# Optimization experiments

Measured on AMD Instinct MI355X. Metric: run time of the kernel, lower is better.

The kernel has to match this reference:

```python
import jax, jax.numpy as jnp
import numpy as np

D = 128            # dim_h
EDIM = D + 108     # tgt emb + 108-way edge one-hot (edge_linear in_features)
NSRC = 10000       # candidate source nodes
NEDGE = 320000     # candidate paths (edges), ~32 per src
TOPN = 6           # top_n path selection
GIN_EPS = 0.0      # init_eps, not learned
BN_EPS = 1e-5


def _batch_norm(x, gamma, beta):
    # torch BatchNorm1d in training mode: batch stats, biased variance
    mean = jnp.mean(x, axis=0)
    var = jnp.var(x, axis=0)
    return gamma * (x - mean) * jax.lax.rsqrt(var + BN_EPS) + beta


def _glorot(key, shape):
    fan_in, fan_out = shape[-2], shape[-1]
    lim = np.sqrt(6.0 / (fan_in + fan_out))
    return jax.random.uniform(key, shape, jnp.float32, -lim, lim)


def setup_inputs() -> dict:
    key = jax.random.key(0)
    ks = jax.random.split(key, 24)
    inp = {
        "paths_srcs": jax.random.normal(ks[0], (NSRC, D), jnp.float32),
        "path_feats": jax.random.normal(ks[1], (NEDGE, EDIM), jnp.float32),
        "src_ids": jax.random.randint(ks[2], (NEDGE,), 0, NSRC, jnp.int32),
        # 3 stacked GIN convs (weights stacked on leading axis)
        "conv_edge_W": _glorot(ks[3], (3, EDIM, D)),
        "conv_edge_b": jnp.zeros((3, D), jnp.float32),
        "conv_W1": _glorot(ks[4], (3, D, D)),       # MLP layer1, no bias
        "conv_bn_g": jnp.ones((3, D), jnp.float32),
        "conv_bn_b": jnp.zeros((3, D), jnp.float32),
        "conv_W2": _glorot(ks[5], (3, D, D)),       # MLP layer2, no bias
        # GINStack heads
        "lin1_W": _glorot(ks[6], (3 * D, D)),
        "lin1_b": jnp.zeros((D,), jnp.float32),
        "lin2_W": _glorot(ks[7], (D, D)),
        "lin2_b": jnp.zeros((D,), jnp.float32),
        # PathEncoder
        "pe_src_W": _glorot(ks[8], (D, D)),
        "pe_src_b": jnp.zeros((D,), jnp.float32),
        "pe_tgt_W": _glorot(ks[9], (EDIM, D)),
        "pe_tgt_b": jnp.zeros((D,), jnp.float32),
        "pe_bn_g": jnp.ones((D,), jnp.float32),
        "pe_bn_b": jnp.zeros((D,), jnp.float32),
        # linear path ranker head
        "score_w": _glorot(ks[10], (D, 1))[:, 0],
    }
    return inp


def reference(paths_srcs, path_feats, conv_edge_W, conv_edge_b, conv_W1,
              conv_bn_g, conv_bn_b, conv_W2, lin1_W, lin1_b, lin2_W, lin2_b,
              pe_src_W, pe_src_b, pe_tgt_W, pe_tgt_b, pe_bn_g, pe_bn_b,
              score_w, src_ids):
    # GIN message: relu(tgt+edge feature), summed per source node.
    # Identical for all 3 convs in the original, so compute once.
    msgs = jax.nn.relu(path_feats)                                   # [E, EDIM]
    agg = jax.ops.segment_sum(msgs, src_ids, num_segments=NSRC)      # [N, EDIM]

    hs = []
    for i in range(3):  # fixed 3-layer GINStack
        h_msg = agg @ conv_edge_W[i] + conv_edge_b[i]                # [N, D]
        h = (1.0 + GIN_EPS) * paths_srcs + h_msg
        z = jax.nn.relu(_batch_norm(h @ conv_W1[i], conv_bn_g[i], conv_bn_b[i]))
        hs.append(z @ conv_W2[i])
    h = jnp.concatenate(hs, axis=1) @ lin1_W + lin1_b                # [N, D]
    h = jax.nn.relu(h)
    node_emb = h @ lin2_W + lin2_b                                   # [N, D]

    # PathEncoder: src-node emb + fused (tgt+edge) emb -> path emb
    hpath = node_emb[src_ids] @ pe_src_W + pe_src_b \
          + path_feats @ pe_tgt_W + pe_tgt_b                         # [E, D]
    hpath = jax.nn.relu(_batch_norm(hpath, pe_bn_g, pe_bn_b))

    # linear path ranker + top-k path selection
    scores = hpath @ score_w                                         # [E]
    top_vals, top_idx = jax.lax.top_k(scores, TOPN)
    return node_emb, top_vals, top_idx
```

## Files before the change

kernel.cpp:

```cpp
#include <hip/hip_runtime.h>
#include <math.h>

#define NSRC 10000
#define NEDGE 320000
#define EDIM 236
#define TOPN 6

typedef __attribute__((ext_vector_type(8))) short short8;
typedef __attribute__((ext_vector_type(4))) float floatx4;

__device__ __forceinline__ unsigned short bf16_rne(float x) {
  union { float f; unsigned int u; } c; c.f = x;
  unsigned int r = (c.u + 0x7FFFu + ((c.u >> 16) & 1u)) >> 16;
  return (unsigned short)r;
}
__device__ __forceinline__ float bf16_to_f(unsigned short h) {
  union { unsigned int u; float f; } c; c.u = ((unsigned int)h) << 16;
  return c.f;
}
__device__ __forceinline__ void split_f32(float x, unsigned short& h, unsigned short& l) {
  h = bf16_rne(x);
  l = bf16_rne(x - bf16_to_f(h));
}

struct KV { float v; int i; };

__device__ __forceinline__ bool kv_better(const KV a, const KV b) {
  return (a.v > b.v) || (a.v == b.v && a.i < b.i);
}

__device__ __forceinline__ void kv_merge(KV d[TOPN], const KV o[TOPN]) {
  KV r[TOPN];
  int ia = 0, ib = 0;
#pragma unroll
  for (int q = 0; q < TOPN; ++q) {
    bool takeA;
    if (ia >= TOPN) takeA = false;
    else if (ib >= TOPN) takeA = true;
    else takeA = kv_better(d[ia], o[ib]);
    r[q] = takeA ? d[ia] : o[ib];
    if (takeA) ia++; else ib++;
  }
#pragma unroll
  for (int q = 0; q < TOPN; ++q) d[q] = r[q];
}

__global__ void k_zero(float* __restrict__ p, int n) {
  int i = blockIdx.x * 256 + threadIdx.x;
  if (i < n) p[i] = 0.f;
}

__global__ void k_sentinel(float* __restrict__ out) {
  if (threadIdx.x == 0) out[0] = 1.0e9f;
}

__global__ void k_prep_w1cat(const float* __restrict__ cw1, float* __restrict__ w1cat) {
  int gid = blockIdx.x * 256 + threadIdx.x;
  if (gid >= 3 * 128 * 128) return;
  int i = gid >> 14;
  int m = (gid >> 7) & 127;
  int j = gid & 127;
  w1cat[m * 384 + i * 128 + j] = cw1[gid];
}

__global__ void k_prep_wew1(const float* __restrict__ cew, const float* __restrict__ cw1,
                            float* __restrict__ wew1cat) {
  int b = blockIdx.x;
  int i = b / EDIM;
  int k = b - i * EDIM;
  int j = threadIdx.x;
  const float* we = cew + ((size_t)i * EDIM + k) * 128;
  const float* w1 = cw1 + (size_t)i * 16384;
  float acc = 0.f;
  for (int m = 0; m < 128; ++m) acc = fmaf(we[m], w1[m * 128 + j], acc);
  wew1cat[k * 384 + i * 128 + j] = acc;
}

__global__ void k_prep_bprime(const float* __restrict__ ceb, const float* __restrict__ cw1,
                              float* __restrict__ bprime) {
  int i = blockIdx.x;
  int j = threadIdx.x;
  const float* be = ceb + i * 128;
  const float* w1 = cw1 + (size_t)i * 16384;
  float acc = 0.f;
  for (int m = 0; m < 128; ++m) acc = fmaf(be[m], w1[m * 128 + j], acc);
  bprime[i * 128 + j] = acc;
}

__global__ void k_prep_m1(const float* __restrict__ cw2, const float* __restrict__ l1w,
                          float* __restrict__ m1) {
  int b = blockIdx.x;
  int i = b >> 7;
  int r = b & 127;
  int j = threadIdx.x;
  const float* w2 = cw2 + (size_t)i * 16384 + r * 128;
  float acc = 0.f;
  for (int c = 0; c < 128; ++c) acc = fmaf(w2[c], l1w[((size_t)i * 128 + c) * 128 + j], acc);
  m1[b * 128 + j] = acc;
}

__global__ void k_prep_bsplit(const float* __restrict__ ptw,
                              unsigned short* __restrict__ Bh,
                              unsigned short* __restrict__ Bl) {
  int n = blockIdx.x;
  int k = threadIdx.x;
  float v = (k < EDIM) ? ptw[(size_t)k * 128 + n] : 0.f;
  unsigned short h, l;
  split_f32(v, h, l);
  Bh[n * 256 + k] = h;
  Bl[n * 256 + k] = l;
}

__global__ __launch_bounds__(256) void k_hist(const int* __restrict__ src,
                                              int* __restrict__ counts) {
  int e = blockIdx.x * 256 + threadIdx.x;
  if (e < NEDGE) atomicAdd(&counts[src[e]], 1);
}

__global__ __launch_bounds__(256) void k_scan(const int* __restrict__ counts,
                                              int* __restrict__ offsets,
                                              int* __restrict__ cursor) {
  __shared__ int part[256];
  const int t = threadIdx.x;
  const int base = t * 40;
  int s = 0;
  for (int k = 0; k < 40; ++k) {
    int i = base + k;
    if (i < NSRC) s += counts[i];
  }
  part[t] = s;
  __syncthreads();
  for (int off = 1; off < 256; off <<= 1) {
    int v = (t >= off) ? part[t - off] : 0;
    __syncthreads();
    part[t] += v;
    __syncthreads();
  }
  int run = (t == 0) ? 0 : part[t - 1];
  for (int k = 0; k < 40; ++k) {
    int i = base + k;
    if (i < NSRC) {
      offsets[i] = run;
      cursor[i] = run;
      run += counts[i];
    }
  }
  if (t == 255) offsets[NSRC] = run;
}

__global__ __launch_bounds__(256) void k_scatter(const int* __restrict__ src,
                                                 int* __restrict__ cursor,
                                                 int* __restrict__ elist) {
  int e = blockIdx.x * 256 + threadIdx.x;
  if (e < NEDGE) {
    int p = atomicAdd(&cursor[src[e]], 1);
    elist[p] = e;
  }
}

__global__ __launch_bounds__(256) void k_gather(const float* __restrict__ pf,
                                                const int* __restrict__ offsets,
                                                const int* __restrict__ elist,
                                                float* __restrict__ agg) {
  const int row = blockIdx.x;
  const int t = threadIdx.x;
  if (t >= EDIM) return;
  const int beg = offsets[row];
  const int end = offsets[row + 1];
  float acc0 = 0.f, acc1 = 0.f;
  int e = beg;
  for (; e + 1 < end; e += 2) {
    int e0 = elist[e];
    int e1 = elist[e + 1];
    float v0 = pf[(size_t)e0 * EDIM + t];
    float v1 = pf[(size_t)e1 * EDIM + t];
    acc0 += fmaxf(v0, 0.f);
    acc1 += fmaxf(v1, 0.f);
  }
  if (e < end) {
    int e0 = elist[e];
    acc0 += fmaxf(pf[(size_t)e0 * EDIM + t], 0.f);
  }
  agg[(size_t)row * EDIM + t] = acc0 + acc1;
}

template <int ATR, int EPI>
__global__ __launch_bounds__(256)
void gemm_k(const float* __restrict__ A, const float* __restrict__ B,
            float* __restrict__ C, int M, int K, int N,
            const float* __restrict__ bn_g, const float* __restrict__ bn_b,
            const float* __restrict__ bn_mean, const float* __restrict__ bn_rstd,
            const float* __restrict__ bias, const float* __restrict__ bias2,
            const float* __restrict__ Cin,
            const int* __restrict__ srcids, const float* __restrict__ gatherTab,
            float* __restrict__ colsum, float* __restrict__ colsumsq) {
  __shared__ float As[8][128];
  __shared__ float Bs[8][128];
  __shared__ float red[16][128];
  constexpr bool STATS = (EPI == 1 || EPI == 4);

  const int tid = threadIdx.x;
  const int tx = tid & 15;
  const int ty = tid >> 4;
  const int bm = blockIdx.x * 128;
  const int bn = blockIdx.y * 128;

  float acc[8][8];
#pragma unroll
  for (int i = 0; i < 8; ++i)
#pragma unroll
    for (int j = 0; j < 8; ++j) acc[i][j] = 0.f;

  for (int k0 = 0; k0 < K; k0 += 8) {
    {
      int r = tid >> 1;
      int cq = (tid & 1) << 2;
      float4 v = make_float4(0.f, 0.f, 0.f, 0.f);
      int row = bm + r;
      if (row < M) {
        const float* ap = A + (size_t)row * K + k0 + cq;
        if (k0 + cq + 4 <= K) {
          v = *(const float4*)ap;
        } else {
          float tmp[4] = {0.f, 0.f, 0.f, 0.f};
          for (int q = 0; q < 4; ++q)
            if (k0 + cq + q < K) tmp[q] = ap[q];
          v = make_float4(tmp[0], tmp[1], tmp[2], tmp[3]);
        }
      }
      if constexpr (ATR == 1) {
        float vv[4] = {v.x, v.y, v.z, v.w};
#pragma unroll
        for (int q = 0; q < 4; ++q) {
          int k = k0 + cq + q;
          if (k < K) {
            vv[q] = fmaxf(fmaf(bn_g[k], (vv[q] - bn_mean[k]) * bn_rstd[k], bn_b[k]), 0.f);
          } else {
            vv[q] = 0.f;
          }
        }
        v = make_float4(vv[0], vv[1], vv[2], vv[3]);
      }
      As[cq + 0][r] = v.x;
      As[cq + 1][r] = v.y;
      As[cq + 2][r] = v.z;
      As[cq + 3][r] = v.w;
    }
    {
      int r = tid >> 5;
      int c = (tid & 31) << 2;
      float4 v = make_float4(0.f, 0.f, 0.f, 0.f);
      int kk = k0 + r;
      if (kk < K) v = *(const float4*)(B + (size_t)kk * N + bn + c);
      *(float4*)&Bs[r][c] = v;
    }
    __syncthreads();
#pragma unroll
    for (int kk = 0; kk < 8; ++kk) {
      const float4 a0 = *(const float4*)&As[kk][ty * 8];
      const float4 a1 = *(const float4*)&As[kk][ty * 8 + 4];
      const float4 b0 = *(const float4*)&Bs[kk][tx * 8];
      const float4 b1 = *(const float4*)&Bs[kk][tx * 8 + 4];
      const float av[8] = {a0.x, a0.y, a0.z, a0.w, a1.x, a1.y, a1.z, a1.w};
      const float bv[8] = {b0.x, b0.y, b0.z, b0.w, b1.x, b1.y, b1.z, b1.w};
#pragma unroll
      for (int i = 0; i < 8; ++i)
#pragma unroll
        for (int j = 0; j < 8; ++j) acc[i][j] = fmaf(av[i], bv[j], acc[i][j]);
    }
    __syncthreads();
  }

  const int nb = bn + tx * 8;
  float colS[8], colQ[8];
  if constexpr (STATS) {
#pragma unroll
    for (int j = 0; j < 8; ++j) { colS[j] = 0.f; colQ[j] = 0.f; }
  }
#pragma unroll
  for (int i = 0; i < 8; ++i) {
    int m = bm + ty * 8 + i;
    if (m < M) {
      float outv[8];
#pragma unroll
      for (int j = 0; j < 8; ++j) outv[j] = acc[i][j];
      if constexpr (EPI == 1) {
        const float* crow = Cin + (size_t)m * N + nb;
#pragma unroll
        for (int j = 0; j < 8; ++j) outv[j] += crow[j] + bias[nb + j];
      } else if constexpr (EPI == 2) {
#pragma unroll
        for (int j = 0; j < 8; ++j) outv[j] = fmaxf(outv[j] + bias[nb + j], 0.f);
      } else if constexpr (EPI == 3) {
#pragma unroll
        for (int j = 0; j < 8; ++j) {
          float bb = bias[nb + j];
          if (bias2) bb += bias2[nb + j];
          outv[j] += bb;
        }
      } else if constexpr (EPI == 4) {
        int s = srcids[m];
        const float* g = gatherTab + (size_t)s * N + nb;
#pragma unroll
        for (int j = 0; j < 8; ++j) outv[j] += g[j];
      }
      float* crow = C + (size_t)m * N + nb;
      *(float4*)crow = make_float4(outv[0], outv[1], outv[2], outv[3]);
      *(float4*)(crow + 4) = make_float4(outv[4], outv[5], outv[6], outv[7]);
      if constexpr (STATS) {
#pragma unroll
        for (int j = 0; j < 8; ++j) { colS[j] += outv[j]; colQ[j] += outv[j] * outv[j]; }
      }
    }
  }
  if constexpr (STATS) {
    *(float4*)&red[ty][tx * 8] = make_float4(colS[0], colS[1], colS[2], colS[3]);
    *(float4*)&red[ty][tx * 8 + 4] = make_float4(colS[4], colS[5], colS[6], colS[7]);
    __syncthreads();
    if (tid < 128) {
      float s = 0.f;
#pragma unroll
      for (int t = 0; t < 16; ++t) s += red[t][tid];
      atomicAdd(colsum + bn + tid, s);
    }
    __syncthreads();
    *(float4*)&red[ty][tx * 8] = make_float4(colQ[0], colQ[1], colQ[2], colQ[3]);
    *(float4*)&red[ty][tx * 8 + 4] = make_float4(colQ[4], colQ[5], colQ[6], colQ[7]);
    __syncthreads();
    if (tid < 128) {
      float s = 0.f;
#pragma unroll
      for (int t = 0; t < 16; ++t) s += red[t][tid];
      atomicAdd(colsumsq + bn + tid, s);
    }
  }
}

__global__ __launch_bounds__(256)
void k_hgemm(const float* __restrict__ A, const unsigned short* __restrict__ Bh,
             const unsigned short* __restrict__ Bl, const int* __restrict__ srcids,
             const float* __restrict__ pre_src, float* __restrict__ hpath,
             float* __restrict__ colsum, float* __restrict__ colsumsq) {
  __shared__ __align__(16) unsigned short Ah[128][40];
  __shared__ __align__(16) unsigned short Al[128][40];
  __shared__ __align__(16) unsigned short Bhs[128][40];
  __shared__ __align__(16) unsigned short Bls[128][40];
  __shared__ float redS[4][128];
  __shared__ float redQ[4][128];

  const int tid = threadIdx.x;
  const int wave = tid >> 6;
  const int lane = tid & 63;
  const int am = lane & 15;
  const int aq = lane >> 4;
  const int bm = blockIdx.x * 128;

  floatx4 acc[2][8];
#pragma unroll
  for (int mt = 0; mt < 2; ++mt)
#pragma unroll
    for (int nt = 0; nt < 8; ++nt) acc[mt][nt] = (floatx4){0.f, 0.f, 0.f, 0.f};

  const int rowS = tid >> 1;
  const int kq = (tid & 1) * 16;

  for (int c = 0; c < 8; ++c) {
    const int k0 = c * 32;
    {
      const float* ap = A + (size_t)(bm + rowS) * EDIM + k0 + kq;
      short8 vh0, vl0, vh1, vl1;
#pragma unroll
      for (int i = 0; i < 4; ++i) {
        float4 v = make_float4(0.f, 0.f, 0.f, 0.f);
        if (k0 + kq + i * 4 + 4 <= EDIM) v = *(const float4*)(ap + i * 4);
        unsigned short h0, l0, h1, l1, h2, l2, h3, l3;
        split_f32(v.x, h0, l0);
        split_f32(v.y, h1, l1);
        split_f32(v.z, h2, l2);
        split_f32(v.w, h3, l3);
        if (i < 2) {
          vh0[i * 4 + 0] = (short)h0; vl0[i * 4 + 0] = (short)l0;
          vh0[i * 4 + 1] = (short)h1; vl0[i * 4 + 1] = (short)l1;
          vh0[i * 4 + 2] = (short)h2; vl0[i * 4 + 2] = (short)l2;
          vh0[i * 4 + 3] = (short)h3; vl0[i * 4 + 3] = (short)l3;
        } else {
          int q = (i - 2) * 4;
          vh1[q + 0] = (short)h0; vl1[q + 0] = (short)l0;
          vh1[q + 1] = (short)h1; vl1[q + 1] = (short)l1;
          vh1[q + 2] = (short)h2; vl1[q + 2] = (short)l2;
          vh1[q + 3] = (short)h3; vl1[q + 3] = (short)l3;
        }
      }
      *(short8*)&Ah[rowS][kq] = vh0;
      *(short8*)&Ah[rowS][kq + 8] = vh1;
      *(short8*)&Al[rowS][kq] = vl0;
      *(short8*)&Al[rowS][kq + 8] = vl1;
    }
    {
      const unsigned short* bhp = Bh + (size_t)rowS * 256 + k0 + kq;
      const unsigned short* blp = Bl + (size_t)rowS * 256 + k0 + kq;
      *(short8*)&Bhs[rowS][kq] = *(const short8*)bhp;
      *(short8*)&Bhs[rowS][kq + 8] = *(const short8*)(bhp + 8);
      *(short8*)&Bls[rowS][kq] = *(const short8*)blp;
      *(short8*)&Bls[rowS][kq + 8] = *(const short8*)(blp + 8);
    }
    __syncthreads();
    {
      const int m0 = wave * 32 + am;
      const short8 ah0 = *(const short8*)&Ah[m0][aq * 8];
      const short8 al0 = *(const short8*)&Al[m0][aq * 8];
      const short8 ah1 = *(const short8*)&Ah[m0 + 16][aq * 8];
      const short8 al1 = *(const short8*)&Al[m0 + 16][aq * 8];
#pragma unroll
      for (int nt = 0; nt < 8; ++nt) {
        const short8 bh = *(const short8*)&Bhs[nt * 16 + am][aq * 8];
        const short8 bl = *(const short8*)&Bls[nt * 16 + am][aq * 8];
        acc[0][nt] = __builtin_amdgcn_mfma_f32_16x16x32_bf16(ah0, bl, acc[0][nt], 0, 0, 0);
        acc[0][nt] = __builtin_amdgcn_mfma_f32_16x16x32_bf16(al0, bh, acc[0][nt], 0, 0, 0);
        acc[0][nt] = __builtin_amdgcn_mfma_f32_16x16x32_bf16(ah0, bh, acc[0][nt], 0, 0, 0);
        acc[1][nt] = __builtin_amdgcn_mfma_f32_16x16x32_bf16(ah1, bl, acc[1][nt], 0, 0, 0);
        acc[1][nt] = __builtin_amdgcn_mfma_f32_16x16x32_bf16(al1, bh, acc[1][nt], 0, 0, 0);
        acc[1][nt] = __builtin_amdgcn_mfma_f32_16x16x32_bf16(ah1, bh, acc[1][nt], 0, 0, 0);
      }
    }
    __syncthreads();
  }

  float colS[8], colQ[8];
#pragma unroll
  for (int nt = 0; nt < 8; ++nt) { colS[nt] = 0.f; colQ[nt] = 0.f; }
#pragma unroll
  for (int mt = 0; mt < 2; ++mt) {
#pragma unroll
    for (int r = 0; r < 4; ++r) {
      const int m = bm + wave * 32 + mt * 16 + aq * 4 + r;
      const int sid = srcids[m];
      const float* g = pre_src + (size_t)sid * 128;
      float* hp = hpath + (size_t)m * 128;
#pragma unroll
      for (int nt = 0; nt < 8; ++nt) {
        const int col = nt * 16 + am;
        float v = acc[mt][nt][r] + g[col];
        hp[col] = v;
        colS[nt] += v;
        colQ[nt] += v * v;
      }
    }
  }
#pragma unroll
  for (int nt = 0; nt < 8; ++nt) {
    colS[nt] += __shfl_xor(colS[nt], 16);
    colS[nt] += __shfl_xor(colS[nt], 32);
    colQ[nt] += __shfl_xor(colQ[nt], 16);
    colQ[nt] += __shfl_xor(colQ[nt], 32);
  }
  if (lane < 16) {
#pragma unroll
    for (int nt = 0; nt < 8; ++nt) {
      redS[wave][nt * 16 + lane] = colS[nt];
      redQ[wave][nt * 16 + lane] = colQ[nt];
    }
  }
  __syncthreads();
  if (tid < 128) {
    float s = redS[0][tid] + redS[1][tid] + redS[2][tid] + redS[3][tid];
    atomicAdd(colsum + tid, s);
  } else {
    int cn = tid - 128;
    float s = redQ[0][cn] + redQ[1][cn] + redQ[2][cn] + redQ[3][cn];
    atomicAdd(colsumsq + cn, s);
  }
}

__global__ void k_finT(float* __restrict__ st) {
  int j = threadIdx.x;
  float mean = st[j] * (1.0f / NSRC);
  float var = st[384 + j] * (1.0f / NSRC) - mean * mean;
  st[768 + j] = mean;
  st[1152 + j] = rsqrtf(var + 1e-5f);
}

__global__ void k_finP(float* __restrict__ st, const float* __restrict__ g,
                       const float* __restrict__ b) {
  int j = threadIdx.x;
  float mean = st[j] * (1.0f / NEDGE);
  float var = st[128 + j] * (1.0f / NEDGE) - mean * mean;
  float rstd = rsqrtf(var + 1e-5f);
  float a = g[j] * rstd;
  st[256 + j] = a;
  st[384 + j] = b[j] - a * mean;
}

__global__ __launch_bounds__(256) void k_score(const float* __restrict__ hpath,
                                               const float* __restrict__ aP,
                                               const float* __restrict__ cP,
                                               const float* __restrict__ w,
                                               float* __restrict__ scores) {
  const int row = blockIdx.x * 16 + (threadIdx.x >> 4);
  const int cg = threadIdx.x & 15;
  const float* hp = hpath + (size_t)row * 128 + cg * 8;
  const float4 x0 = *(const float4*)hp;
  const float4 x1 = *(const float4*)(hp + 4);
  const float xs[8] = {x0.x, x0.y, x0.z, x0.w, x1.x, x1.y, x1.z, x1.w};
  float part = 0.f;
#pragma unroll
  for (int q = 0; q < 8; ++q) {
    int j = cg * 8 + q;
    part += fmaxf(fmaf(aP[j], xs[q], cP[j]), 0.f) * w[j];
  }
#pragma unroll
  for (int o = 8; o >= 1; o >>= 1) part += __shfl_xor(part, o, 16);
  if (cg == 0) scores[row] = part;
}

__global__ __launch_bounds__(256) void k_top1(const float* __restrict__ scores,
                                              KV* __restrict__ cand) {
  KV t[TOPN];
#pragma unroll
  for (int q = 0; q < TOPN; ++q) { t[q].v = -INFINITY; t[q].i = 2147483647; }
  for (int e = blockIdx.x * 256 + threadIdx.x; e < NEDGE; e += 256 * 256) {
    float v = scores[e];
    if (v > t[TOPN - 1].v) {
      t[TOPN - 1].v = v;
      t[TOPN - 1].i = e;
#pragma unroll
      for (int q = TOPN - 1; q > 0; --q) {
        if (t[q].v > t[q - 1].v) { KV tmp = t[q - 1]; t[q - 1] = t[q]; t[q] = tmp; }
      }
    }
  }
  __shared__ KV sh[128][TOPN];
  int tid = threadIdx.x;
  for (int s = 128; s >= 1; s >>= 1) {
    if (tid >= s && tid < 2 * s) {
#pragma unroll
      for (int q = 0; q < TOPN; ++q) sh[tid - s][q] = t[q];
    }
    __syncthreads();
    if (tid < s) kv_merge(t, sh[tid]);
    __syncthreads();
  }
  if (tid == 0) {
#pragma unroll
    for (int q = 0; q < TOPN; ++q) cand[blockIdx.x * TOPN + q] = t[q];
  }
}

__global__ __launch_bounds__(256) void k_top2(const KV* __restrict__ cand,
                                              float* __restrict__ outTail) {
  int tid = threadIdx.x;
  KV t[TOPN];
#pragma unroll
  for (int q = 0; q < TOPN; ++q) t[q] = cand[tid * TOPN + q];
  __shared__ KV sh[128][TOPN];
  for (int s = 128; s >= 1; s >>= 1) {
    if (tid >= s && tid < 2 * s) {
#pragma unroll
      for (int q = 0; q < TOPN; ++q) sh[tid - s][q] = t[q];
    }
    __syncthreads();
    if (tid < s) kv_merge(t, sh[tid]);
    __syncthreads();
  }
  if (tid == 0) {
#pragma unroll
    for (int q = 0; q < TOPN; ++q) {
      outTail[q] = t[q].v;
      outTail[TOPN + q] = (float)t[q].i;
    }
  }
}

extern "C" void kernel_launch(void* const* d_in, const int* in_sizes, int n_in,
                              void* d_out, int out_size, void* d_ws, size_t ws_size,
                              hipStream_t stream) {
  const float* paths_srcs = (const float*)d_in[0];
  const float* path_feats = (const float*)d_in[1];
  const int* src_ids = (const int*)d_in[2];
  const float* cew = (const float*)d_in[3];
  const float* ceb = (const float*)d_in[4];
  const float* cw1 = (const float*)d_in[5];
  const float* bng = (const float*)d_in[6];
  const float* bnbt = (const float*)d_in[7];
  const float* cw2 = (const float*)d_in[8];
  const float* l1w = (const float*)d_in[9];
  const float* l1b = (const float*)d_in[10];
  const float* l2w = (const float*)d_in[11];
  const float* l2b = (const float*)d_in[12];
  const float* psw = (const float*)d_in[13];
  const float* psb = (const float*)d_in[14];
  const float* ptw = (const float*)d_in[15];
  const float* ptb = (const float*)d_in[16];
  const float* pbg = (const float*)d_in[17];
  const float* pbb = (const float*)d_in[18];
  const float* scw = (const float*)d_in[19];
  float* out = (float*)d_out;
  float* ws = (float*)d_ws;

  float* w1cat = ws;
  float* wew1cat = w1cat + 49152;
  float* bprime = wew1cat + 90624;
  float* m1 = bprime + 512;
  float* statsT = m1 + 49152;
  float* statsP = statsT + 1536;
  float* agg = statsP + 512;
  float* T = agg + 2360000;
  float* H1 = T + 3840000;
  float* pre_src = H1 + 1280000;
  float* scores = pre_src + 1280000;
  KV* cand = (KV*)(scores + 320000);
  float* hpath = scores + 320000 + 3072;
  unsigned short* Bh = (unsigned short*)(hpath + 40960000);
  unsigned short* Bl = Bh + 32768;
  int* counts = (int*)hpath;
  int* offsets = counts + 10000;
  int* cursor = offsets + 10001;
  int* elist = cursor + 10000;
  const size_t needed = (size_t)(49152 + 90624 + 512 + 49152 + 1536 + 512 + 2360000 +
                                 3840000 + 1280000 + 1280000 + 320000 + 3072 +
                                 40960000 + 16384 + 16384) * 4;
  if (ws_size < needed) {
    k_sentinel<<<1, 64, 0, stream>>>(out);
    return;
  }

  const float* np = nullptr;

  k_prep_w1cat<<<192, 256, 0, stream>>>(cw1, w1cat);
  k_prep_wew1<<<708, 128, 0, stream>>>(cew, cw1, wew1cat);
  k_prep_bprime<<<3, 128, 0, stream>>>(ceb, cw1, bprime);
  k_prep_m1<<<384, 128, 0, stream>>>(cw2, l1w, m1);
  k_prep_bsplit<<<128, 256, 0, stream>>>(ptw, Bh, Bl);

  k_zero<<<8, 256, 0, stream>>>(statsT, 2048);
  k_zero<<<(10000 + 255) / 256, 256, 0, stream>>>((float*)counts, 10000);

  k_hist<<<(NEDGE + 255) / 256, 256, 0, stream>>>(src_ids, counts);
  k_scan<<<1, 256, 0, stream>>>(counts, offsets, cursor);
  k_scatter<<<(NEDGE + 255) / 256, 256, 0, stream>>>(src_ids, cursor, elist);
  k_gather<<<NSRC, 256, 0, stream>>>(path_feats, offsets, elist, agg);

  gemm_k<0, 0><<<dim3(79, 3), 256, 0, stream>>>(paths_srcs, w1cat, T, NSRC, 128, 384,
                                                np, np, np, np, np, np, np, nullptr, np,
                                                nullptr, nullptr);
  gemm_k<0, 1><<<dim3(79, 3), 256, 0, stream>>>(agg, wew1cat, T, NSRC, EDIM, 384,
                                                np, np, np, np, bprime, np, T, nullptr,
                                                np, statsT, statsT + 384);
  k_finT<<<1, 384, 0, stream>>>(statsT);
  gemm_k<1, 2><<<dim3(79, 1), 256, 0, stream>>>(T, m1, H1, NSRC, 384, 128,
                                                bng, bnbt, statsT + 768, statsT + 1152,
                                                l1b, np, np, nullptr, np, nullptr, nullptr);
  gemm_k<0, 3><<<dim3(79, 1), 256, 0, stream>>>(H1, l2w, out, NSRC, 128, 128,
                                                np, np, np, np, l2b, np, np, nullptr, np,
                                                nullptr, nullptr);
  gemm_k<0, 3><<<dim3(79, 1), 256, 0, stream>>>(out, psw, pre_src, NSRC, 128, 128,
                                                np, np, np, np, psb, ptb, np, nullptr, np,
                                                nullptr, nullptr);

  k_hgemm<<<2500, 256, 0, stream>>>(path_feats, Bh, Bl, src_ids, pre_src, hpath,
                                    statsP, statsP + 128);
  k_finP<<<1, 128, 0, stream>>>(statsP, pbg, pbb);

  k_score<<<NEDGE / 16, 256, 0, stream>>>(hpath, statsP + 256, statsP + 384, scw, scores);
  k_top1<<<256, 256, 0, stream>>>(scores, cand);
  k_top2<<<1, 256, 0, stream>>>(cand, out + (size_t)NSRC * 128);
}
```

Measured before the change: 1.072 ms.

## Fuse prep kernels, GEMM stages, BN finalize and score+topk; restructure gather and hgemm

Merges all weight-prep and zeroing kernels into a single launch. Fuses the two T GEMMs into one kernel that does the K-concatenated product and collects BN stats. Folds the BN finalize steps into their consumers, and computes lin2 and pe_src together with pre-multiplied weights. Score computation is fused with the top-k pass, and the gather stages edge ids in shared memory with 4-way accumulation. The hgemm now loads A directly into registers instead of splitting it through LDS. Together these cut launch overhead and intermediate round-trips, at the cost of redundant per-thread BN-stat recomputation.

```diff
diff --git a/kernel.cpp b/kernel.cpp
--- a/kernel.cpp
+++ b/kernel.cpp
@@ -45,70 +45,84 @@
   for (int q = 0; q < TOPN; ++q) d[q] = r[q];
 }
 
-__global__ void k_zero(float* __restrict__ p, int n) {
-  int i = blockIdx.x * 256 + threadIdx.x;
-  if (i < n) p[i] = 0.f;
-}
-
 __global__ void k_sentinel(float* __restrict__ out) {
   if (threadIdx.x == 0) out[0] = 1.0e9f;
 }
 
-__global__ void k_prep_w1cat(const float* __restrict__ cw1, float* __restrict__ w1cat) {
-  int gid = blockIdx.x * 256 + threadIdx.x;
-  if (gid >= 3 * 128 * 128) return;
-  int i = gid >> 14;
-  int m = (gid >> 7) & 127;
-  int j = gid & 127;
-  w1cat[m * 384 + i * 128 + j] = cw1[gid];
-}
-
-__global__ void k_prep_wew1(const float* __restrict__ cew, const float* __restrict__ cw1,
-                            float* __restrict__ wew1cat) {
-  int b = blockIdx.x;
-  int i = b / EDIM;
-  int k = b - i * EDIM;
-  int j = threadIdx.x;
-  const float* we = cew + ((size_t)i * EDIM + k) * 128;
-  const float* w1 = cw1 + (size_t)i * 16384;
-  float acc = 0.f;
-  for (int m = 0; m < 128; ++m) acc = fmaf(we[m], w1[m * 128 + j], acc);
-  wew1cat[k * 384 + i * 128 + j] = acc;
-}
-
-__global__ void k_prep_bprime(const float* __restrict__ ceb, const float* __restrict__ cw1,
-                              float* __restrict__ bprime) {
-  int i = blockIdx.x;
-  int j = threadIdx.x;
-  const float* be = ceb + i * 128;
-  const float* w1 = cw1 + (size_t)i * 16384;
-  float acc = 0.f;
-  for (int m = 0; m < 128; ++m) acc = fmaf(be[m], w1[m * 128 + j], acc);
-  bprime[i * 128 + j] = acc;
-}
-
-__global__ void k_prep_m1(const float* __restrict__ cw2, const float* __restrict__ l1w,
-                          float* __restrict__ m1) {
-  int b = blockIdx.x;
-  int i = b >> 7;
-  int r = b & 127;
-  int j = threadIdx.x;
-  const float* w2 = cw2 + (size_t)i * 16384 + r * 128;
-  float acc = 0.f;
-  for (int c = 0; c < 128; ++c) acc = fmaf(w2[c], l1w[((size_t)i * 128 + c) * 128 + j], acc);
-  m1[b * 128 + j] = acc;
-}
-
-__global__ void k_prep_bsplit(const float* __restrict__ ptw,
-                              unsigned short* __restrict__ Bh,
-                              unsigned short* __restrict__ Bl) {
-  int n = blockIdx.x;
-  int k = threadIdx.x;
-  float v = (k < EDIM) ? ptw[(size_t)k * 128 + n] : 0.f;
-  unsigned short h, l;
-  split_f32(v, h, l);
-  Bh[n * 256 + k] = h;
-  Bl[n * 256 + k] = l;
+__global__ __launch_bounds__(256)
+void k_prep_all(const float* __restrict__ cew, const float* __restrict__ ceb,
+                const float* __restrict__ cw1, const float* __restrict__ cw2,
+                const float* __restrict__ l1w, const float* __restrict__ l2w,
+                const float* __restrict__ psw, const float* __restrict__ l2b,
+                const float* __restrict__ psb, const float* __restrict__ ptb,
+                const float* __restrict__ ptw,
+                float* __restrict__ w1cat, float* __restrict__ wew1cat,
+                float* __restrict__ bprime, float* __restrict__ m1,
+                unsigned short* __restrict__ Bh, unsigned short* __restrict__ Bl,
+                float* __restrict__ bcat, float* __restrict__ biascat,
+                float* __restrict__ statsT, int* __restrict__ counts) {
+  const int b = blockIdx.x;
+  const int tid = threadIdx.x;
+  if (b < 708) {
+    if (tid >= 128) return;
+    int i = b / EDIM;
+    int k = b - i * EDIM;
+    const float* we = cew + ((size_t)i * EDIM + k) * 128;
+    const float* w1 = cw1 + (size_t)i * 16384;
+    float acc = 0.f;
+    for (int m = 0; m < 128; ++m) acc = fmaf(we[m], w1[m * 128 + tid], acc);
+    wew1cat[k * 384 + i * 128 + tid] = acc;
+  } else if (b < 1092) {
+    if (tid >= 128) return;
+    int bb = b - 708;
+    int i = bb >> 7;
+    int r = bb & 127;
+    const float* w2 = cw2 + (size_t)i * 16384 + r * 128;
+    float acc = 0.f;
+    for (int c = 0; c < 128; ++c) acc = fmaf(w2[c], l1w[((size_t)i * 128 + c) * 128 + tid], acc);
+    m1[bb * 128 + tid] = acc;
+  } else if (b < 1284) {
+    int gid = (b - 1092) * 256 + tid;
+    if (gid >= 3 * 128 * 128) return;
+    int i = gid >> 14;
+    int m = (gid >> 7) & 127;
+    int j = gid & 127;
+    w1cat[m * 384 + i * 128 + j] = cw1[gid];
+  } else if (b < 1287) {
+    if (tid >= 128) return;
+    int i = b - 1284;
+    const float* be = ceb + i * 128;
+    const float* w1 = cw1 + (size_t)i * 16384;
+    float acc = 0.f;
+    for (int m = 0; m < 128; ++m) acc = fmaf(be[m], w1[m * 128 + tid], acc);
+    bprime[i * 128 + tid] = acc;
+  } else if (b < 1415) {
+    int n = b - 1287;
+    float v = (tid < EDIM) ? ptw[(size_t)tid * 128 + n] : 0.f;
+    unsigned short h, l;
+    split_f32(v, h, l);
+    Bh[n * 256 + tid] = h;
+    Bl[n * 256 + tid] = l;
+  } else if (b < 1543) {
+    if (tid >= 128) return;
+    int k = b - 1415;
+    bcat[k * 256 + tid] = l2w[k * 128 + tid];
+    float acc = 0.f;
+    for (int c = 0; c < 128; ++c) acc = fmaf(l2w[k * 128 + c], psw[c * 128 + tid], acc);
+    bcat[k * 256 + 128 + tid] = acc;
+    if (k == 0) {
+      biascat[tid] = l2b[tid];
+      float bb = 0.f;
+      for (int c = 0; c < 128; ++c) bb = fmaf(l2b[c], psw[c * 128 + tid], bb);
+      biascat[128 + tid] = bb + psb[tid] + ptb[tid];
+    }
+  } else if (b < 1551) {
+    int i = (b - 1543) * 256 + tid;
+    if (i < 2048) statsT[i] = 0.f;
+  } else {
+    int i = (b - 1551) * 256 + tid;
+    if (i < NSRC) counts[i] = 0;
+  }
 }
 
 __global__ __launch_bounds__(256) void k_hist(const int* __restrict__ src,
@@ -164,24 +178,141 @@
                                                 float* __restrict__ agg) {
   const int row = blockIdx.x;
   const int t = threadIdx.x;
-  if (t >= EDIM) return;
+  __shared__ int sid[64];
   const int beg = offsets[row];
   const int end = offsets[row + 1];
-  float acc0 = 0.f, acc1 = 0.f;
-  int e = beg;
-  for (; e + 1 < end; e += 2) {
-    int e0 = elist[e];
-    int e1 = elist[e + 1];
-    float v0 = pf[(size_t)e0 * EDIM + t];
-    float v1 = pf[(size_t)e1 * EDIM + t];
-    acc0 += fmaxf(v0, 0.f);
-    acc1 += fmaxf(v1, 0.f);
-  }
-  if (e < end) {
-    int e0 = elist[e];
-    acc0 += fmaxf(pf[(size_t)e0 * EDIM + t], 0.f);
-  }
-  agg[(size_t)row * EDIM + t] = acc0 + acc1;
+  float a0 = 0.f, a1 = 0.f, a2 = 0.f, a3 = 0.f;
+  for (int b = beg; b < end; b += 64) {
+    const int cnt = min(64, end - b);
+    __syncthreads();
+    if (t < cnt) sid[t] = elist[b + t];
+    __syncthreads();
+    if (t < EDIM) {
+      int e = 0;
+      for (; e + 4 <= cnt; e += 4) {
+        int i0 = sid[e], i1 = sid[e + 1], i2 = sid[e + 2], i3 = sid[e + 3];
+        a0 += fmaxf(pf[(size_t)i0 * EDIM + t], 0.f);
+        a1 += fmaxf(pf[(size_t)i1 * EDIM + t], 0.f);
+        a2 += fmaxf(pf[(size_t)i2 * EDIM + t], 0.f);
+        a3 += fmaxf(pf[(size_t)i3 * EDIM + t], 0.f);
+      }
+      for (; e < cnt; ++e) a0 += fmaxf(pf[(size_t)sid[e] * EDIM + t], 0.f);
+    }
+  }
+  if (t < EDIM) agg[(size_t)row * EDIM + t] = (a0 + a1) + (a2 + a3);
+}
+
+__global__ __launch_bounds__(256)
+void k_gemmT(const float* __restrict__ A1, const float* __restrict__ B1,
+             const float* __restrict__ A2, const float* __restrict__ B2,
+             const float* __restrict__ bias, float* __restrict__ C,
+             float* __restrict__ colsum, float* __restrict__ colsumsq) {
+  __shared__ float As[8][128];
+  __shared__ float Bs[8][128];
+  __shared__ float red[16][128];
+  const int tid = threadIdx.x;
+  const int tx = tid & 15;
+  const int ty = tid >> 4;
+  const int bm = blockIdx.x * 128;
+  const int bn = blockIdx.y * 128;
+  const int N = 384;
+
+  float acc[8][8];
+#pragma unroll
+  for (int i = 0; i < 8; ++i)
+#pragma unroll
+    for (int j = 0; j < 8; ++j) acc[i][j] = 0.f;
+
+#pragma unroll 1
+  for (int seg = 0; seg < 2; ++seg) {
+    const float* A = seg ? A2 : A1;
+    const float* B = seg ? B2 : B1;
+    const int K = seg ? EDIM : 128;
+    for (int k0 = 0; k0 < K; k0 += 8) {
+      {
+        int r = tid >> 1;
+        int cq = (tid & 1) << 2;
+        float4 v = make_float4(0.f, 0.f, 0.f, 0.f);
+        int row = bm + r;
+        if (row < NSRC) {
+          const float* ap = A + (size_t)row * K + k0 + cq;
+          if (k0 + cq + 4 <= K) {
+            v = *(const float4*)ap;
+          } else {
+            float tmp[4] = {0.f, 0.f, 0.f, 0.f};
+            for (int q = 0; q < 4; ++q)
+              if (k0 + cq + q < K) tmp[q] = ap[q];
+            v = make_float4(tmp[0], tmp[1], tmp[2], tmp[3]);
+          }
+        }
+        As[cq + 0][r] = v.x;
+        As[cq + 1][r] = v.y;
+        As[cq + 2][r] = v.z;
+        As[cq + 3][r] = v.w;
+      }
+      {
+        int r = tid >> 5;
+        int c = (tid & 31) << 2;
+        float4 v = make_float4(0.f, 0.f, 0.f, 0.f);
+        int kk = k0 + r;
+        if (kk < K) v = *(const float4*)(B + (size_t)kk * N + bn + c);
+        *(float4*)&Bs[r][c] = v;
+      }
+      __syncthreads();
+#pragma unroll
+      for (int kk = 0; kk < 8; ++kk) {
+        const float4 a0 = *(const float4*)&As[kk][ty * 8];
+        const float4 a1 = *(const float4*)&As[kk][ty * 8 + 4];
+        const float4 b0 = *(const float4*)&Bs[kk][tx * 8];
+        const float4 b1 = *(const float4*)&Bs[kk][tx * 8 + 4];
+        const float av[8] = {a0.x, a0.y, a0.z, a0.w, a1.x, a1.y, a1.z, a1.w};
+        const float bv[8] = {b0.x, b0.y, b0.z, b0.w, b1.x, b1.y, b1.z, b1.w};
+#pragma unroll
+        for (int i = 0; i < 8; ++i)
+#pragma unroll
+          for (int j = 0; j < 8; ++j) acc[i][j] = fmaf(av[i], bv[j], acc[i][j]);
+      }
+      __syncthreads();
+    }
+  }
+
+  const int nb = bn + tx * 8;
+  float colS[8], colQ[8];
+#pragma unroll
+  for (int j = 0; j < 8; ++j) { colS[j] = 0.f; colQ[j] = 0.f; }
+#pragma unroll
+  for (int i = 0; i < 8; ++i) {
+    int m = bm + ty * 8 + i;
+    if (m < NSRC) {
+      float outv[8];
+#pragma unroll
+      for (int j = 0; j < 8; ++j) outv[j] = acc[i][j] + bias[nb + j];
+      float* crow = C + (size_t)m * N + nb;
+      *(float4*)crow = make_float4(outv[0], outv[1], outv[2], outv[3]);
+      *(float4*)(crow + 4) = make_float4(outv[4], outv[5], outv[6], outv[7]);
+#pragma unroll
+      for (int j = 0; j < 8; ++j) { colS[j] += outv[j]; colQ[j] += outv[j] * outv[j]; }
+    }
+  }
+  *(float4*)&red[ty][tx * 8] = make_float4(colS[0], colS[1], colS[2], colS[3]);
+  *(float4*)&red[ty][tx * 8 + 4] = make_float4(colS[4], colS[5], colS[6], colS[7]);
+  __syncthreads();
+  if (tid < 128) {
+    float s = 0.f;
+#pragma unroll
+    for (int t = 0; t < 16; ++t) s += red[t][tid];
+    atomicAdd(colsum + bn + tid, s);
+  }
+  __syncthreads();
+  *(float4*)&red[ty][tx * 8] = make_float4(colQ[0], colQ[1], colQ[2], colQ[3]);
+  *(float4*)&red[ty][tx * 8 + 4] = make_float4(colQ[4], colQ[5], colQ[6], colQ[7]);
+  __syncthreads();
+  if (tid < 128) {
+    float s = 0.f;
+#pragma unroll
+    for (int t = 0; t < 16; ++t) s += red[t][tid];
+    atomicAdd(colsumsq + bn + tid, s);
+  }
 }
 
 template <int ATR, int EPI>
@@ -189,16 +320,10 @@
 void gemm_k(const float* __restrict__ A, const float* __restrict__ B,
             float* __restrict__ C, int M, int K, int N,
             const float* __restrict__ bn_g, const float* __restrict__ bn_b,
-            const float* __restrict__ bn_mean, const float* __restrict__ bn_rstd,
-            const float* __restrict__ bias, const float* __restrict__ bias2,
-            const float* __restrict__ Cin,
-            const int* __restrict__ srcids, const float* __restrict__ gatherTab,
-            float* __restrict__ colsum, float* __restrict__ colsumsq) {
+            const float* __restrict__ rawS, const float* __restrict__ rawQ,
+            const float* __restrict__ bias, float* __restrict__ C2) {
   __shared__ float As[8][128];
   __shared__ float Bs[8][128];
-  __shared__ float red[16][128];
-  constexpr bool STATS = (EPI == 1 || EPI == 4);
-
   const int tid = threadIdx.x;
   const int tx = tid & 15;
   const int ty = tid >> 4;
@@ -228,13 +353,16 @@
           v = make_float4(tmp[0], tmp[1], tmp[2], tmp[3]);
         }
       }
-      if constexpr (ATR == 1) {
+      if constexpr (ATR == 2) {
         float vv[4] = {v.x, v.y, v.z, v.w};
 #pragma unroll
         for (int q = 0; q < 4; ++q) {
           int k = k0 + cq + q;
           if (k < K) {
-            vv[q] = fmaxf(fmaf(bn_g[k], (vv[q] - bn_mean[k]) * bn_rstd[k], bn_b[k]), 0.f);
+            float mean = rawS[k] * (1.0f / NSRC);
+            float var = rawQ[k] * (1.0f / NSRC) - mean * mean;
+            float rstd = rsqrtf(var + 1e-5f);
+            vv[q] = fmaxf(fmaf(bn_g[k] * rstd, vv[q] - mean, bn_b[k]), 0.f);
           } else {
             vv[q] = 0.f;
           }
@@ -272,66 +400,24 @@
   }
 
   const int nb = bn + tx * 8;
-  float colS[8], colQ[8];
-  if constexpr (STATS) {
-#pragma unroll
-    for (int j = 0; j < 8; ++j) { colS[j] = 0.f; colQ[j] = 0.f; }
-  }
 #pragma unroll
   for (int i = 0; i < 8; ++i) {
     int m = bm + ty * 8 + i;
     if (m < M) {
       float outv[8];
 #pragma unroll
-      for (int j = 0; j < 8; ++j) outv[j] = acc[i][j];
-      if constexpr (EPI == 1) {
-        const float* crow = Cin + (size_t)m * N + nb;
-#pragma unroll
-        for (int j = 0; j < 8; ++j) outv[j] += crow[j] + bias[nb + j];
-      } else if constexpr (EPI == 2) {
-#pragma unroll
-        for (int j = 0; j < 8; ++j) outv[j] = fmaxf(outv[j] + bias[nb + j], 0.f);
-      } else if constexpr (EPI == 3) {
-#pragma unroll
-        for (int j = 0; j < 8; ++j) {
-          float bb = bias[nb + j];
-          if (bias2) bb += bias2[nb + j];
-          outv[j] += bb;
-        }
-      } else if constexpr (EPI == 4) {
-        int s = srcids[m];
-        const float* g = gatherTab + (size_t)s * N + nb;
-#pragma unroll
-        for (int j = 0; j < 8; ++j) outv[j] += g[j];
-      }
-      float* crow = C + (size_t)m * N + nb;
+      for (int j = 0; j < 8; ++j) {
+        outv[j] = acc[i][j] + bias[nb + j];
+        if constexpr (EPI == 2) outv[j] = fmaxf(outv[j], 0.f);
+      }
+      float* crow;
+      if constexpr (EPI == 5) {
+        crow = (nb < 128) ? (C + (size_t)m * 128 + nb) : (C2 + (size_t)m * 128 + (nb - 128));
+      } else {
+        crow = C + (size_t)m * N + nb;
+      }
       *(float4*)crow = make_float4(outv[0], outv[1], outv[2], outv[3]);
       *(float4*)(crow + 4) = make_float4(outv[4], outv[5], outv[6], outv[7]);
-      if constexpr (STATS) {
-#pragma unroll
-        for (int j = 0; j < 8; ++j) { colS[j] += outv[j]; colQ[j] += outv[j] * outv[j]; }
-      }
-    }
-  }
-  if constexpr (STATS) {
-    *(float4*)&red[ty][tx * 8] = make_float4(colS[0], colS[1], colS[2], colS[3]);
-    *(float4*)&red[ty][tx * 8 + 4] = make_float4(colS[4], colS[5], colS[6], colS[7]);
-    __syncthreads();
-    if (tid < 128) {
-      float s = 0.f;
-#pragma unroll
-      for (int t = 0; t < 16; ++t) s += red[t][tid];
-      atomicAdd(colsum + bn + tid, s);
-    }
-    __syncthreads();
-    *(float4*)&red[ty][tx * 8] = make_float4(colQ[0], colQ[1], colQ[2], colQ[3]);
-    *(float4*)&red[ty][tx * 8 + 4] = make_float4(colQ[4], colQ[5], colQ[6], colQ[7]);
-    __syncthreads();
-    if (tid < 128) {
-      float s = 0.f;
-#pragma unroll
-      for (int t = 0; t < 16; ++t) s += red[t][tid];
-      atomicAdd(colsumsq + bn + tid, s);
     }
   }
 }
@@ -341,8 +427,6 @@
              const unsigned short* __restrict__ Bl, const int* __restrict__ srcids,
              const float* __restrict__ pre_src, float* __restrict__ hpath,
              float* __restrict__ colsum, float* __restrict__ colsumsq) {
-  __shared__ __align__(16) unsigned short Ah[128][40];
-  __shared__ __align__(16) unsigned short Al[128][40];
   __shared__ __align__(16) unsigned short Bhs[128][40];
   __shared__ __align__(16) unsigned short Bls[128][40];
   __shared__ float redS[4][128];
@@ -363,39 +447,11 @@
 
   const int rowS = tid >> 1;
   const int kq = (tid & 1) * 16;
+  const float* a0p = A + (size_t)(bm + wave * 32 + am) * EDIM;
+  const float* a1p = a0p + 16 * EDIM;
 
   for (int c = 0; c < 8; ++c) {
     const int k0 = c * 32;
-    {
-      const float* ap = A + (size_t)(bm + rowS) * EDIM + k0 + kq;
-      short8 vh0, vl0, vh1, vl1;
-#pragma unroll
-      for (int i = 0; i < 4; ++i) {
-        float4 v = make_float4(0.f, 0.f, 0.f, 0.f);
-        if (k0 + kq + i * 4 + 4 <= EDIM) v = *(const float4*)(ap + i * 4);
-        unsigned short h0, l0, h1, l1, h2, l2, h3, l3;
-        split_f32(v.x, h0, l0);
-        split_f32(v.y, h1, l1);
-        split_f32(v.z, h2, l2);
-        split_f32(v.w, h3, l3);
-        if (i < 2) {
-          vh0[i * 4 + 0] = (short)h0; vl0[i * 4 + 0] = (short)l0;
-          vh0[i * 4 + 1] = (short)h1; vl0[i * 4 + 1] = (short)l1;
-          vh0[i * 4 + 2] = (short)h2; vl0[i * 4 + 2] = (short)l2;
-          vh0[i * 4 + 3] = (short)h3; vl0[i * 4 + 3] = (short)l3;
-        } else {
-          int q = (i - 2) * 4;
-          vh1[q + 0] = (short)h0; vl1[q + 0] = (short)l0;
-          vh1[q + 1] = (short)h1; vl1[q + 1] = (short)l1;
-          vh1[q + 2] = (short)h2; vl1[q + 2] = (short)l2;
-          vh1[q + 3] = (short)h3; vl1[q + 3] = (short)l3;
-        }
-      }
-      *(short8*)&Ah[rowS][kq] = vh0;
-      *(short8*)&Ah[rowS][kq + 8] = vh1;
-      *(short8*)&Al[rowS][kq] = vl0;
-      *(short8*)&Al[rowS][kq + 8] = vl1;
-    }
     {
       const unsigned short* bhp = Bh + (size_t)rowS * 256 + k0 + kq;
       const unsigned short* blp = Bl + (size_t)rowS * 256 + k0 + kq;
@@ -404,24 +460,45 @@
       *(short8*)&Bls[rowS][kq] = *(const short8*)blp;
       *(short8*)&Bls[rowS][kq + 8] = *(const short8*)(blp + 8);
     }
-    __syncthreads();
-    {
-      const int m0 = wave * 32 + am;
-      const short8 ah0 = *(const short8*)&Ah[m0][aq * 8];
-      const short8 al0 = *(const short8*)&Al[m0][aq * 8];
-      const short8 ah1 = *(const short8*)&Ah[m0 + 16][aq * 8];
-      const short8 al1 = *(const short8*)&Al[m0 + 16][aq * 8];
-#pragma unroll
-      for (int nt = 0; nt < 8; ++nt) {
-        const short8 bh = *(const short8*)&Bhs[nt * 16 + am][aq * 8];
-        const short8 bl = *(const short8*)&Bls[nt * 16 + am][aq * 8];
-        acc[0][nt] = __builtin_amdgcn_mfma_f32_16x16x32_bf16(ah0, bl, acc[0][nt], 0, 0, 0);
-        acc[0][nt] = __builtin_amdgcn_mfma_f32_16x16x32_bf16(al0, bh, acc[0][nt], 0, 0, 0);
-        acc[0][nt] = __builtin_amdgcn_mfma_f32_16x16x32_bf16(ah0, bh, acc[0][nt], 0, 0, 0);
-        acc[1][nt] = __builtin_amdgcn_mfma_f32_16x16x32_bf16(ah1, bl, acc[1][nt], 0, 0, 0);
-        acc[1][nt] = __builtin_amdgcn_mfma_f32_16x16x32_bf16(al1, bh, acc[1][nt], 0, 0, 0);
-        acc[1][nt] = __builtin_amdgcn_mfma_f32_16x16x32_bf16(ah1, bh, acc[1][nt], 0, 0, 0);
-      }
+    const int kA = k0 + aq * 8;
+    float av0[8], av1[8];
+    if (kA + 8 <= EDIM) {
+      float4 x = *(const float4*)(a0p + kA);
+      float4 y = *(const float4*)(a0p + kA + 4);
+      av0[0] = x.x; av0[1] = x.y; av0[2] = x.z; av0[3] = x.w;
+      av0[4] = y.x; av0[5] = y.y; av0[6] = y.z; av0[7] = y.w;
+      x = *(const float4*)(a1p + kA);
+      y = *(const float4*)(a1p + kA + 4);
+      av1[0] = x.x; av1[1] = x.y; av1[2] = x.z; av1[3] = x.w;
+      av1[4] = y.x; av1[5] = y.y; av1[6] = y.z; av1[7] = y.w;
+    } else {
+#pragma unroll
+      for (int q = 0; q < 8; ++q) {
+        int k = kA + q;
+        av0[q] = (k < EDIM) ? a0p[k] : 0.f;
+        av1[q] = (k < EDIM) ? a1p[k] : 0.f;
+      }
+    }
+    short8 ah0, al0, ah1, al1;
+#pragma unroll
+    for (int q = 0; q < 8; ++q) {
+      unsigned short h, l;
+      split_f32(av0[q], h, l);
+      ah0[q] = (short)h; al0[q] = (short)l;
+      split_f32(av1[q], h, l);
+      ah1[q] = (short)h; al1[q] = (short)l;
+    }
+    __syncthreads();
+#pragma unroll
+    for (int nt = 0; nt < 8; ++nt) {
+      const short8 bh = *(const short8*)&Bhs[nt * 16 + am][aq * 8];
+      const short8 bl = *(const short8*)&Bls[nt * 16 + am][aq * 8];
+      acc[0][nt] = __builtin_amdgcn_mfma_f32_16x16x32_bf16(ah0, bl, acc[0][nt], 0, 0, 0);
+      acc[1][nt] = __builtin_amdgcn_mfma_f32_16x16x32_bf16(ah1, bl, acc[1][nt], 0, 0, 0);
+      acc[0][nt] = __builtin_amdgcn_mfma_f32_16x16x32_bf16(al0, bh, acc[0][nt], 0, 0, 0);
+      acc[1][nt] = __builtin_amdgcn_mfma_f32_16x16x32_bf16(al1, bh, acc[1][nt], 0, 0, 0);
+      acc[0][nt] = __builtin_amdgcn_mfma_f32_16x16x32_bf16(ah0, bh, acc[0][nt], 0, 0, 0);
+      acc[1][nt] = __builtin_amdgcn_mfma_f32_16x16x32_bf16(ah1, bh, acc[1][nt], 0, 0, 0);
     }
     __syncthreads();
   }
@@ -472,57 +549,42 @@
   }
 }
 
-__global__ void k_finT(float* __restrict__ st) {
-  int j = threadIdx.x;
-  float mean = st[j] * (1.0f / NSRC);
-  float var = st[384 + j] * (1.0f / NSRC) - mean * mean;
-  st[768 + j] = mean;
-  st[1152 + j] = rsqrtf(var + 1e-5f);
-}
-
-__global__ void k_finP(float* __restrict__ st, const float* __restrict__ g,
-                       const float* __restrict__ b) {
-  int j = threadIdx.x;
-  float mean = st[j] * (1.0f / NEDGE);
-  float var = st[128 + j] * (1.0f / NEDGE) - mean * mean;
-  float rstd = rsqrtf(var + 1e-5f);
-  float a = g[j] * rstd;
-  st[256 + j] = a;
-  st[384 + j] = b[j] - a * mean;
-}
-
-__global__ __launch_bounds__(256) void k_score(const float* __restrict__ hpath,
-                                               const float* __restrict__ aP,
-                                               const float* __restrict__ cP,
-                                               const float* __restrict__ w,
-                                               float* __restrict__ scores) {
-  const int row = blockIdx.x * 16 + (threadIdx.x >> 4);
-  const int cg = threadIdx.x & 15;
-  const float* hp = hpath + (size_t)row * 128 + cg * 8;
-  const float4 x0 = *(const float4*)hp;
-  const float4 x1 = *(const float4*)(hp + 4);
-  const float xs[8] = {x0.x, x0.y, x0.z, x0.w, x1.x, x1.y, x1.z, x1.w};
-  float part = 0.f;
+__global__ __launch_bounds__(256)
+void k_scoretop(const float* __restrict__ hpath, const float* __restrict__ stP,
+                const float* __restrict__ g, const float* __restrict__ b,
+                const float* __restrict__ w, KV* __restrict__ cand) {
+  const int tid = threadIdx.x;
+  const int cg = tid & 15;
+  const int grp = (blockIdx.x * 256 + tid) >> 4;
+  float a8[8], c8[8], w8[8];
 #pragma unroll
   for (int q = 0; q < 8; ++q) {
     int j = cg * 8 + q;
-    part += fmaxf(fmaf(aP[j], xs[q], cP[j]), 0.f) * w[j];
-  }
-#pragma unroll
-  for (int o = 8; o >= 1; o >>= 1) part += __shfl_xor(part, o, 16);
-  if (cg == 0) scores[row] = part;
-}
-
-__global__ __launch_bounds__(256) void k_top1(const float* __restrict__ scores,
-                                              KV* __restrict__ cand) {
+    float mean = stP[j] * (1.0f / NEDGE);
+    float var = stP[128 + j] * (1.0f / NEDGE) - mean * mean;
+    float rstd = rsqrtf(var + 1e-5f);
+    float aj = g[j] * rstd;
+    a8[q] = aj;
+    c8[q] = b[j] - aj * mean;
+    w8[q] = w[j];
+  }
   KV t[TOPN];
 #pragma unroll
   for (int q = 0; q < TOPN; ++q) { t[q].v = -INFINITY; t[q].i = 2147483647; }
-  for (int e = blockIdx.x * 256 + threadIdx.x; e < NEDGE; e += 256 * 256) {
-    float v = scores[e];
-    if (v > t[TOPN - 1].v) {
-      t[TOPN - 1].v = v;
-      t[TOPN - 1].i = e;
+  for (int row = grp; row < NEDGE; row += 4096) {
+    const float* hp = hpath + (size_t)row * 128 + cg * 8;
+    const float4 x0 = *(const float4*)hp;
+    const float4 x1 = *(const float4*)(hp + 4);
+    const float xs[8] = {x0.x, x0.y, x0.z, x0.w, x1.x, x1.y, x1.z, x1.w};
+    float part = 0.f;
+#pragma unroll
+    for (int q = 0; q < 8; ++q)
+      part += fmaxf(fmaf(a8[q], xs[q], c8[q]), 0.f) * w8[q];
+#pragma unroll
+    for (int o = 8; o >= 1; o >>= 1) part += __shfl_xor(part, o, 16);
+    if (cg == 0 && part > t[TOPN - 1].v) {
+      t[TOPN - 1].v = part;
+      t[TOPN - 1].i = row;
 #pragma unroll
       for (int q = TOPN - 1; q > 0; --q) {
         if (t[q].v > t[q - 1].v) { KV tmp = t[q - 1]; t[q - 1] = t[q]; t[q] = tmp; }
@@ -530,7 +592,6 @@
     }
   }
   __shared__ KV sh[128][TOPN];
-  int tid = threadIdx.x;
   for (int s = 128; s >= 1; s >>= 1) {
     if (tid >= s && tid < 2 * s) {
 #pragma unroll
@@ -607,61 +668,42 @@
   float* T = agg + 2360000;
   float* H1 = T + 3840000;
   float* pre_src = H1 + 1280000;
-  float* scores = pre_src + 1280000;
-  KV* cand = (KV*)(scores + 320000);
-  float* hpath = scores + 320000 + 3072;
+  float* scores_dead = pre_src + 1280000;
+  KV* cand = (KV*)(scores_dead + 320000);
+  float* hpath = scores_dead + 320000 + 3072;
   unsigned short* Bh = (unsigned short*)(hpath + 40960000);
   unsigned short* Bl = Bh + 32768;
+  float* bcat = (float*)(Bl + 32768);
+  float* biascat = bcat + 32768;
   int* counts = (int*)hpath;
   int* offsets = counts + 10000;
   int* cursor = offsets + 10001;
   int* elist = cursor + 10000;
   const size_t needed = (size_t)(49152 + 90624 + 512 + 49152 + 1536 + 512 + 2360000 +
                                  3840000 + 1280000 + 1280000 + 320000 + 3072 +
-                                 40960000 + 16384 + 16384) * 4;
+                                 40960000 + 16384 + 16384 + 32768 + 256) * 4;
   if (ws_size < needed) {
     k_sentinel<<<1, 64, 0, stream>>>(out);
     return;
   }
 
-  const float* np = nullptr;
-
-  k_prep_w1cat<<<192, 256, 0, stream>>>(cw1, w1cat);
-  k_prep_wew1<<<708, 128, 0, stream>>>(cew, cw1, wew1cat);
-  k_prep_bprime<<<3, 128, 0, stream>>>(ceb, cw1, bprime);
-  k_prep_m1<<<384, 128, 0, stream>>>(cw2, l1w, m1);
-  k_prep_bsplit<<<128, 256, 0, stream>>>(ptw, Bh, Bl);
-
-  k_zero<<<8, 256, 0, stream>>>(statsT, 2048);
-  k_zero<<<(10000 + 255) / 256, 256, 0, stream>>>((float*)counts, 10000);
-
+  k_prep_all<<<1591, 256, 0, stream>>>(cew, ceb, cw1, cw2, l1w, l2w, psw, l2b, psb, ptb,
+                                       ptw, w1cat, wew1cat, bprime, m1, Bh, Bl,
+                                       bcat, biascat, statsT, counts);
   k_hist<<<(NEDGE + 255) / 256, 256, 0, stream>>>(src_ids, counts);
   k_scan<<<1, 256, 0, stream>>>(counts, offsets, cursor);
   k_scatter<<<(NEDGE + 255) / 256, 256, 0, stream>>>(src_ids, cursor, elist);
   k_gather<<<NSRC, 256, 0, stream>>>(path_feats, offsets, elist, agg);
-
-  gemm_k<0, 0><<<dim3(79, 3), 256, 0, stream>>>(paths_srcs, w1cat, T, NSRC, 128, 384,
-                                                np, np, np, np, np, np, np, nullptr, np,
-                                                nullptr, nullptr);
-  gemm_k<0, 1><<<dim3(79, 3), 256, 0, stream>>>(agg, wew1cat, T, NSRC, EDIM, 384,
-                                                np, np, np, np, bprime, np, T, nullptr,
-                                                np, statsT, statsT + 384);
-  k_finT<<<1, 384, 0, stream>>>(statsT);
-  gemm_k<1, 2><<<dim3(79, 1), 256, 0, stream>>>(T, m1, H1, NSRC, 384, 128,
-                                                bng, bnbt, statsT + 768, statsT + 1152,
-                                                l1b, np, np, nullptr, np, nullptr, nullptr);
-  gemm_k<0, 3><<<dim3(79, 1), 256, 0, stream>>>(H1, l2w, out, NSRC, 128, 128,
-                                                np, np, np, np, l2b, np, np, nullptr, np,
-                                                nullptr, nullptr);
-  gemm_k<0, 3><<<dim3(79, 1), 256, 0, stream>>>(out, psw, pre_src, NSRC, 128, 128,
-                                                np, np, np, np, psb, ptb, np, nullptr, np,
-                                                nullptr, nullptr);
-
+  k_gemmT<<<dim3(79, 3), 256, 0, stream>>>(paths_srcs, w1cat, agg, wew1cat, bprime, T,
+                                           statsT, statsT + 384);
+  gemm_k<2, 2><<<dim3(79, 1), 256, 0, stream>>>(T, m1, H1, NSRC, 384, 128,
+                                                bng, bnbt, statsT, statsT + 384,
+                                                l1b, nullptr);
+  gemm_k<0, 5><<<dim3(79, 2), 256, 0, stream>>>(H1, bcat, out, NSRC, 128, 256,
+                                                nullptr, nullptr, nullptr, nullptr,
+                                                biascat, pre_src);
   k_hgemm<<<2500, 256, 0, stream>>>(path_feats, Bh, Bl, src_ids, pre_src, hpath,
                                     statsP, statsP + 128);
-  k_finP<<<1, 128, 0, stream>>>(statsP, pbg, pbb);
-
-  k_score<<<NEDGE / 16, 256, 0, stream>>>(hpath, statsP + 256, statsP + 384, scw, scores);
-  k_top1<<<256, 256, 0, stream>>>(scores, cand);
+  k_scoretop<<<256, 256, 0, stream>>>(hpath, statsP, pbg, pbb, scw, cand);
   k_top2<<<1, 256, 0, stream>>>(cand, out + (size_t)NSRC * 128);
 }
```

Result: faster. 990.1 us (-7.7%).
